# Kernel optimization log

Measured on AMD Instinct MI355X. Metric: run time of the kernel, lower is better.

The kernel has to match this reference:

```python
import jax, jax.numpy as jnp
import numpy as np

B, S, H = 1, 2048, 1024
NH, HD = 16, 64
WIN = 512
M_MEM, M_PER = 512, 64
SCALE = 1.0 / np.sqrt(HD)
NEG_INF = jnp.float32(-1e30)


def setup_inputs() -> dict:
    key = jax.random.key(0)
    ks = jax.random.split(key, 22)
    std = 1.0 / np.sqrt(H)
    def w(k):
        return (jax.random.normal(k, (H, H), jnp.float32) * std)
    names = ['local_wq','local_wk','local_wv','local_wo',
             'long_wq','long_wk','long_wv','long_wo',
             'mem_wq','mem_wk','mem_wv','mem_wo',
             'per_wq','per_wk','per_wv','per_wo']
    d = {n: w(ks[i]) for i, n in enumerate(names)}
    d['gate_w'] = jax.random.normal(ks[16], (4 * H, 4), jnp.float32) * 0.02
    d['gate_b'] = jnp.zeros((4,), jnp.float32)
    d['x'] = jax.random.normal(ks[17], (B, S, H), jnp.float32)
    d['memory_kv'] = jax.random.normal(ks[18], (B, M_MEM, H), jnp.float32)
    d['persona_kv'] = jax.random.normal(ks[19], (B, M_PER, H), jnp.float32)
    return d


def _split_heads(t):
    # (B, T, H) -> (B, NH, T, HD)
    b, t_, _ = t.shape
    return t.reshape(b, t_, NH, HD).transpose(0, 2, 1, 3)


def _merge_heads(t):
    b, h, t_, d = t.shape
    return t.transpose(0, 2, 1, 3).reshape(b, t_, h * d)


def _self_attn(x, wq, wk, wv, wo, mask):
    # mask: (S, S) bool, True = masked out
    q = _split_heads(x @ wq)
    k = _split_heads(x @ wk)
    v = _split_heads(x @ wv)
    scores = jnp.einsum('bhsd,bhtd->bhst', q, k) * SCALE
    scores = jnp.where(mask[None, None], NEG_INF, scores)
    a = jax.nn.softmax(scores, axis=-1)
    out = jnp.einsum('bhst,bhtd->bhsd', a, v)
    return _merge_heads(out) @ wo


def _cross_attn(x, ctx, wq, wk, wv, wo):
    q = _split_heads(x @ wq)
    k = _split_heads(ctx @ wk)
    v = _split_heads(ctx @ wv)
    scores = jnp.einsum('bhsd,bhmd->bhsm', q, k) * SCALE
    a = jax.nn.softmax(scores, axis=-1)
    out = jnp.einsum('bhsm,bhmd->bhsd', a, v)
    return _merge_heads(out) @ wo


def reference(x, memory_kv, persona_kv,
              local_wq, local_wk, local_wv, local_wo,
              long_wq, long_wk, long_wv, long_wo,
              mem_wq, mem_wk, mem_wv, mem_wo,
              per_wq, per_wk, per_wv, per_wo,
              gate_w, gate_b):
    s = x.shape[1]
    idx = jnp.arange(s)
    causal = idx[None, :] > idx[:, None]                    # future tokens masked
    local = causal | ((idx[:, None] - idx[None, :]) > WIN)  # sliding window + causal

    local_out = _self_attn(x, local_wq, local_wk, local_wv, local_wo, local)
    long_out = _self_attn(x, long_wq, long_wk, long_wv, long_wo, causal)
    mem_out = _cross_attn(x, memory_kv, mem_wq, mem_wk, mem_wv, mem_wo)
    per_out = _cross_attn(x, persona_kv, per_wq, per_wk, per_wv, per_wo)

    outs = (local_out, long_out, mem_out, per_out)
    gate_in = jnp.concatenate(outs, axis=-1)                # (B, S, 4H)
    gates = jax.nn.softmax(gate_in @ gate_w + gate_b, axis=-1)  # (B, S, 4)
    fused = sum(gates[..., i:i + 1] * o for i, o in enumerate(outs))
    return fused  # emotion_scale = 1.0, dropout off (eval)
```

## Files before the change

### kernel.cpp

```cpp
#include <hip/hip_runtime.h>

#define S 2048
#define H 1024
#define NH 16
#define HD 64
#define WIN 512
#define SCALE_Q 0.18033688f
#define SM_SHIFT 16.0f

typedef unsigned short u16;
typedef unsigned int u32;
typedef __attribute__((ext_vector_type(8))) short bfrag;
typedef __attribute__((ext_vector_type(4))) float facc;
typedef __attribute__((ext_vector_type(4))) unsigned short u16x4;

#define VMCNT(n) asm volatile("s_waitcnt vmcnt(" #n ")" ::: "memory")

constexpr size_t M1    = 1u << 20;
constexpr size_t WTO   = 0;
constexpr size_t XBO   = 8 * M1;
constexpr size_t MEMBO = 10 * M1;
constexpr size_t PERBO = MEMBO + (M1 >> 1);
constexpr size_t QO    = PERBO + (M1 >> 4);
constexpr size_t KVO   = QO + 8 * M1;
constexpr size_t K2O   = KVO + 8 * M1;
constexpr size_t V2O   = K2O + (M1 >> 1);
constexpr size_t K3O   = V2O + (M1 >> 1);
constexpr size_t V3O   = K3O + (M1 >> 4);
constexpr size_t VT1O  = V3O + (M1 >> 4);
constexpr size_t VT2O  = VT1O + 2 * M1;
constexpr size_t VT3O  = VT2O + (M1 >> 1);
constexpr size_t RECSZ16 = 9216;

__device__ __forceinline__ u16 f2bf(float f) {
    union { float f; unsigned u; } v; v.f = f;
    unsigned r = v.u + 0x7fffu + ((v.u >> 16) & 1u);
    return (u16)(r >> 16);
}
__device__ __forceinline__ float bf2f(u16 b) {
    union { unsigned u; float f; } v; v.u = ((unsigned)b) << 16;
    return v.f;
}
__device__ __forceinline__ void gload16(const u16* g, u16* l) {
    __builtin_amdgcn_global_load_lds(
        (const __attribute__((address_space(1))) u32*)g,
        (__attribute__((address_space(3))) u32*)l, 16, 0, 0);
}
__device__ __forceinline__ u32 cvt_pk(float a, float b) {
    u32 w;
    asm("v_cvt_pk_bf16_f32 %0, %1, %2" : "=v"(w) : "v"(a), "v"(b));
    return w;
}
__device__ __forceinline__ void blockbar() {
    __builtin_amdgcn_sched_barrier(0);
    asm volatile("" ::: "memory");
    __builtin_amdgcn_s_barrier();
    asm volatile("" ::: "memory");
    __builtin_amdgcn_sched_barrier(0);
}

__global__ __launch_bounds__(256)
void cast_all(const float* __restrict__ x, const float* __restrict__ mem,
              const float* __restrict__ per, u16* __restrict__ ws) {
    int i = blockIdx.x * 256 + threadIdx.x;
    const float* src; u16* dst;
    if (i < 262144)           { src = x;   dst = ws + XBO;   }
    else if (i < 327680)      { src = mem; dst = ws + MEMBO; i -= 262144; }
    else if (i < 335872)      { src = per; dst = ws + PERBO; i -= 327680; }
    else return;
    const float4* p = reinterpret_cast<const float4*>(src) + (size_t)i * 2;
    float4 a = p[0], b = p[1];
    u16x4 o0, o1;
    o0[0] = f2bf(a.x); o0[1] = f2bf(a.y); o0[2] = f2bf(a.z); o0[3] = f2bf(a.w);
    o1[0] = f2bf(b.x); o1[1] = f2bf(b.y); o1[2] = f2bf(b.z); o1[3] = f2bf(b.w);
    u16x4* q = reinterpret_cast<u16x4*>(dst) + (size_t)i * 2;
    q[0] = o0; q[1] = o1;
}

__global__ __launch_bounds__(256)
void transp_cast8(const float* __restrict__ w0, const float* __restrict__ w1,
                  const float* __restrict__ w2, const float* __restrict__ w3,
                  const float* __restrict__ w4, const float* __restrict__ w5,
                  const float* __restrict__ w6, const float* __restrict__ w7,
                  u16* __restrict__ wt) {
    __shared__ float t[64][65];
    const float* wp[8] = {w0, w1, w2, w3, w4, w5, w6, w7};
    const float* w = wp[blockIdx.z];
    u16* o = wt + (size_t)blockIdx.z * (1024 * 1024);
    const int kt = blockIdx.y * 64, nt = blockIdx.x * 64;
    const int r = threadIdx.x >> 4, c4 = (threadIdx.x & 15) * 4;
#pragma unroll
    for (int p = 0; p < 4; p++) {
        float4 v = *reinterpret_cast<const float4*>(
            &w[(size_t)(kt + r + p * 16) * 1024 + nt + c4]);
        t[r + p * 16][c4 + 0] = v.x; t[r + p * 16][c4 + 1] = v.y;
        t[r + p * 16][c4 + 2] = v.z; t[r + p * 16][c4 + 3] = v.w;
    }
    __syncthreads();
#pragma unroll
    for (int p = 0; p < 4; p++) {
        int nn = r + p * 16;
        u16x4 ov;
        ov[0] = f2bf(t[c4 + 0][nn]); ov[1] = f2bf(t[c4 + 1][nn]);
        ov[2] = f2bf(t[c4 + 2][nn]); ov[3] = f2bf(t[c4 + 3][nn]);
        *reinterpret_cast<u16x4*>(&o[(size_t)(nt + nn) * 1024 + kt + c4]) = ov;
    }
}

__global__ __launch_bounds__(256)
void transp_v(u16* __restrict__ ws) {
    const int z = blockIdx.z;
    const int Skv = (z < 2) ? 2048 : (z == 2 ? 512 : 64);
    const int kb = blockIdx.x;
    if (kb * 64 >= Skv) return;
    const int h = blockIdx.y;
    const u16* V = ws + (z == 0 ? KVO + 2 * M1 : z == 1 ? KVO + 6 * M1
                       : z == 2 ? V2O : V3O);
    u16* VT = ws + (z == 0 ? XBO : z == 1 ? VT1O : z == 2 ? VT2O : VT3O);
    __shared__ __align__(16) u16 t[64][72];
    {
        const int r = threadIdx.x >> 3, c8 = (threadIdx.x & 7) * 8;
#pragma unroll
        for (int p = 0; p < 2; p++) {
            int rr = r + p * 32;
            bfrag v = *reinterpret_cast<const bfrag*>(
                &V[(size_t)(kb * 64 + rr) * 1024 + h * 64 + c8]);
            *reinterpret_cast<bfrag*>(&t[rr][c8]) = v;
        }
    }
    __syncthreads();
    {
        const int d = threadIdx.x & 63;
        const int k8b = (threadIdx.x >> 6) * 8;
#pragma unroll
        for (int p = 0; p < 2; p++) {
            int k8 = k8b + p * 32;
            bfrag o;
#pragma unroll
            for (int j = 0; j < 8; j++) o[j] = (short)t[k8 + j][d];
            *reinterpret_cast<bfrag*>(
                &VT[(size_t)(h * 64 + d) * Skv + kb * 64 + k8]) = o;
        }
    }
}

__global__ __launch_bounds__(512, 2)
void gemm256(const u16* __restrict__ A, const u16* __restrict__ Bt,
             u16* __restrict__ C, long sB, long sC, int scaleMask) {
    __shared__ __align__(16) u16 sa[2][256 * 64];
    __shared__ __align__(16) u16 sb[2][256 * 64];
    Bt += (size_t)blockIdx.z * sB;
    C  += (size_t)blockIdx.z * sC;
    const float scl = ((scaleMask >> blockIdx.z) & 1) ? SCALE_Q : 1.0f;
    const int tid = threadIdx.x;
    const int wid = tid >> 6, lane = tid & 63;
    const int lhi = lane >> 4, llo = lane & 15;
    const int wm = wid >> 2, wn = wid & 3;
    const int row0 = blockIdx.y * 256, col0 = blockIdx.x * 256;

    facc acc[8][4];
#pragma unroll
    for (int i = 0; i < 8; i++)
#pragma unroll
        for (int j = 0; j < 4; j++)
#pragma unroll
            for (int k = 0; k < 4; k++) acc[i][j][k] = 0.f;

    auto stageB = [&](int kt, int h) {
        const int b = kt & 1, k0 = kt * 64;
#pragma unroll
        for (int pass = 0; pass < 2; pass++) {
            int i = pass * 512 + tid;
            int r = h * 128 + (i >> 3);
            int ck = (i & 7) ^ (r & 7);
            gload16(&Bt[(size_t)(col0 + r) * 1024 + k0 + ck * 8],
                    &sb[b][(size_t)(h * 1024 + pass * 512 + wid * 64) * 8]);
        }
    };
    auto stageAg = [&](int kt, int g) {
        const int b = kt & 1, k0 = kt * 64;
#pragma unroll
        for (int pass = 0; pass < 2; pass++) {
            int i = pass * 512 + tid;
            int i8 = i >> 3;
            int r = g * 64 + (i8 & 63) + (i8 >> 6) * 128;
            int ck = (i & 7) ^ (r & 7);
            int b8 = (pass * 512 + wid * 64) >> 3;
            int rb = g * 64 + (b8 & 63) + (b8 >> 6) * 128;
            gload16(&A[(size_t)(row0 + r) * 1024 + k0 + ck * 8],
                    &sa[b][(size_t)rb * 64]);
        }
    };

    stageB(0, 0); stageB(0, 1); stageAg(0, 0); stageAg(0, 1);
    __builtin_amdgcn_sched_barrier(0);
    VMCNT(2);
    blockbar();

    for (int j = 0; j < 16; j++) {
        const int b = j & 1;
        const u16* pa = &sa[b][0];
        const u16* pb = &sb[b][0];
        bfrag bf[4][2];
#pragma unroll
        for (int q = 0; q < 4; q++) {
            if (q == 0) {
#pragma unroll
                for (int nf = 0; nf < 4; nf++)
#pragma unroll
                    for (int ks = 0; ks < 2; ks++) {
                        int r = wn * 64 + nf * 16 + llo;
                        int p = (ks * 4 + lhi) ^ (r & 7);
                        bf[nf][ks] = *reinterpret_cast<const bfrag*>(
                            &pb[r * 64 + p * 8]);
                    }
            }
            bfrag af[2][2];
#pragma unroll
            for (int rr = 0; rr < 2; rr++)
#pragma unroll
                for (int ks = 0; ks < 2; ks++) {
                    int r = wm * 128 + (q * 2 + rr) * 16 + llo;
                    int p = (ks * 4 + lhi) ^ (r & 7);
                    af[rr][ks] = *reinterpret_cast<const bfrag*>(
                        &pa[r * 64 + p * 8]);
                }
            if (j < 15) {
                if (q == 0)      stageB(j + 1, 0);
                else if (q == 1) stageB(j + 1, 1);
                else if (q == 2) stageAg(j + 1, 0);
                else             stageAg(j + 1, 1);
            }
            blockbar();
            asm volatile("s_waitcnt lgkmcnt(0)" ::: "memory");
            __builtin_amdgcn_sched_barrier(0);
            __builtin_amdgcn_s_setprio(1);
#pragma unroll
            for (int rr = 0; rr < 2; rr++)
#pragma unroll
                for (int nf = 0; nf < 4; nf++)
#pragma unroll
                    for (int ks = 0; ks < 2; ks++)
                        acc[q * 2 + rr][nf] = __builtin_amdgcn_mfma_f32_16x16x32_bf16(
                            af[rr][ks], bf[nf][ks], acc[q * 2 + rr][nf], 0, 0, 0);
            __builtin_amdgcn_s_setprio(0);
            __builtin_amdgcn_sched_barrier(0);
            if (q == 1) { if (j < 15) { VMCNT(4); } else { VMCNT(0); } }
            else if (q == 3 && j < 15) { VMCNT(2); }
            blockbar();
        }
    }

#pragma unroll
    for (int mf = 0; mf < 8; mf++) {
#pragma unroll
        for (int r = 0; r < 4; r++) {
            int row = row0 + wm * 128 + mf * 16 + lhi * 4 + r;
#pragma unroll
            for (int nf = 0; nf < 4; nf++) {
                int col = col0 + wn * 64 + nf * 16 + llo;
                C[(size_t)row * 1024 + col] = f2bf(acc[mf][nf][r] * scl);
            }
        }
    }
}

__device__ __forceinline__ void gemm128_body(
    const u16* __restrict__ A, const u16* __restrict__ Bt, u16* __restrict__ C,
    int M, float scl, u16* sa, u16* sb, int row0, int col0) {
    const int tid = threadIdx.x;
    const int wid = tid >> 6, lane = tid & 63;
    const int lhi = lane >> 4, llo = lane & 15;
    const int wm = wid >> 1, wn = wid & 1;

    facc acc[4][4];
#pragma unroll
    for (int i = 0; i < 4; i++)
#pragma unroll
        for (int j = 0; j < 4; j++)
#pragma unroll
            for (int k = 0; k < 4; k++) acc[i][j][k] = 0.f;

    const int srow = lane >> 3, schunk = lane & 7;
    for (int kt = 0; kt < 16; kt++) {
        __syncthreads();
        const int k0 = kt * 64;
#pragma unroll
        for (int j = 0; j < 4; j++) {
            int r = wid * 32 + j * 8 + srow;
            int ck = schunk ^ (r & 7);
            int ar = row0 + r; if (ar > M - 1) ar = M - 1;
            gload16(&A[(size_t)ar * 1024 + k0 + ck * 8], &sa[(wid * 4 + j) * 512]);
            gload16(&Bt[(size_t)(col0 + r) * 1024 + k0 + ck * 8], &sb[(wid * 4 + j) * 512]);
        }
        __syncthreads();
#pragma unroll
        for (int ks = 0; ks < 2; ks++) {
            bfrag af[4], bfv[4];
#pragma unroll
            for (int mf = 0; mf < 4; mf++) {
                int r = wm * 64 + mf * 16 + llo;
                int p = (ks * 4 + lhi) ^ (r & 7);
                af[mf] = *reinterpret_cast<const bfrag*>(&sa[r * 64 + p * 8]);
            }
#pragma unroll
            for (int nf = 0; nf < 4; nf++) {
                int r = wn * 64 + nf * 16 + llo;
                int p = (ks * 4 + lhi) ^ (r & 7);
                bfv[nf] = *reinterpret_cast<const bfrag*>(&sb[r * 64 + p * 8]);
            }
            __builtin_amdgcn_s_setprio(1);
#pragma unroll
            for (int mf = 0; mf < 4; mf++)
#pragma unroll
                for (int nf = 0; nf < 4; nf++)
                    acc[mf][nf] = __builtin_amdgcn_mfma_f32_16x16x32_bf16(
                        af[mf], bfv[nf], acc[mf][nf], 0, 0, 0);
            __builtin_amdgcn_s_setprio(0);
        }
    }
#pragma unroll
    for (int mf = 0; mf < 4; mf++) {
#pragma unroll
        for (int r = 0; r < 4; r++) {
            int row = row0 + wm * 64 + mf * 16 + lhi * 4 + r;
            if (row < M) {
#pragma unroll
                for (int nf = 0; nf < 4; nf++) {
                    int col = col0 + wn * 64 + nf * 16 + llo;
                    C[(size_t)row * 1024 + col] = f2bf(acc[mf][nf][r] * scl);
                }
            }
        }
    }
}

__global__ __launch_bounds__(256)
void gemm_bf16(const u16* __restrict__ A, const u16* __restrict__ Bt,
               u16* __restrict__ C, int M, long sA, long sB, long sC,
               int scaleMask) {
    __shared__ __align__(16) u16 sa[128 * 64];
    __shared__ __align__(16) u16 sb[128 * 64];
    A  += (size_t)blockIdx.z * sA;
    Bt += (size_t)blockIdx.z * sB;
    C  += (size_t)blockIdx.z * sC;
    const float scl = ((scaleMask >> blockIdx.z) & 1) ? SCALE_Q : 1.0f;
    gemm128_body(A, Bt, C, M, scl, sa, sb, blockIdx.y * 128, blockIdx.x * 128);
}

__global__ __launch_bounds__(256)
void gemm_small(u16* __restrict__ ws) {
    const int z = blockIdx.z;
    if (z >= 2 && blockIdx.y > 0) return;
    __shared__ __align__(16) u16 sa[128 * 64];
    __shared__ __align__(16) u16 sb[128 * 64];
    const u16* A = ws + ((z < 2) ? MEMBO : PERBO);
    const int M = (z < 2) ? 512 : 64;
    const u16* Bt = ws + WTO + (size_t)z * M1;
    u16* C = ws + (z == 0 ? K2O : z == 1 ? V2O : z == 2 ? K3O : V3O);
    gemm128_body(A, Bt, C, M, 1.0f, sa, sb, blockIdx.y * 128, blockIdx.x * 128);
}

__global__ __launch_bounds__(256)
void attn_tiled(u16* __restrict__ ws) {
    __shared__ __align__(16) u16 ksm[2][64 * 64];
    __shared__ __align__(16) u16 vtm[2][64 * 64];
    __shared__ __align__(16) u16 psm[4][16][72];

    const int blk = blockIdx.x;
    int branch, h, qb, piece = 0, nway = 1, rid = -1;
    if (blk < 256)        { branch = 0; qb = 15 - (blk >> 4); h = blk & 15; }
    else if (blk < 768)   { branch = 1; int i = blk - 256; qb = 15 - (i >> 6);
                            int t = i & 63; h = t >> 2; piece = t & 3; nway = 4;
                            rid = h * 40 + 8 + (qb - 8) * 4 + piece; }
    else if (blk < 896)   { branch = 1; int i = blk - 768; qb = 7 - (i >> 5);
                            int t = i & 31; h = t >> 1; piece = t & 1; nway = 2;
                            rid = h * 40 + (qb - 4) * 2 + piece; }
    else if (blk < 960)   { branch = 1; int i = blk - 896; qb = 3 - (i >> 4); h = i & 15; }
    else if (blk < 1216)  { branch = 2; int i = blk - 960; qb = i >> 4; h = i & 15; }
    else                  { branch = 3; int i = blk - 1216; qb = i >> 4; h = i & 15; }
    const bool partial = (rid >= 0);

    size_t kb_, vb_; int Skv, maskMode;
    if (branch == 0)      { kb_ = KVO;          vb_ = XBO;  Skv = 2048; maskMode = 2; }
    else if (branch == 1) { kb_ = KVO + 4 * M1; vb_ = VT1O; Skv = 2048; maskMode = 1; }
    else if (branch == 2) { kb_ = K2O;          vb_ = VT2O; Skv = 512;  maskMode = 0; }
    else                  { kb_ = K3O;          vb_ = VT3O; Skv = 64;   maskMode = 0; }
    const u16* Kp  = ws + kb_;
    const u16* VTp = ws + vb_;
    u16* Qp = ws + QO + (size_t)branch * 2 * M1;

    const int tid = threadIdx.x, wid = tid >> 6, lane = tid & 63;
    const int llo = lane & 15, lhi = lane >> 4;
    const int q0 = qb * 128;
    const int qw = q0 + wid * 32;
    const int hoff = h * 64;

    int tBeg, tEnd;
    if (branch == 1) {
        int n = qb * 2 + 2;
        tBeg = (n * piece) / nway;
        tEnd = (n * (piece + 1)) / nway;
    } else if (branch == 0) {
        tEnd = qb * 2 + 2;
        tBeg = (q0 >= WIN) ? ((q0 - WIN) >> 6) : 0;
    } else {
        tBeg = 0; tEnd = Skv >> 6;
    }
    int myBeg = tBeg, myEnd = tEnd;
    if (maskMode) { int e = ((qw + 31) >> 6) + 1; if (e < myEnd) myEnd = e; }
    if (maskMode == 2 && qw >= WIN) { int b = (qw - WIN) >> 6; if (b > myBeg) myBeg = b; }

    bfrag qf[2][2];
#pragma unroll
    for (int sub = 0; sub < 2; sub++)
#pragma unroll
        for (int ds = 0; ds < 2; ds++)
            qf[sub][ds] = *reinterpret_cast<const bfrag*>(
                &Qp[(size_t)(qw + sub * 16 + llo) * 1024 + hoff + ds * 32 + lhi * 8]);

    facc ot[2][4];
    float lsum[2] = {0.f, 0.f};
#pragma unroll
    for (int sub = 0; sub < 2; sub++)
#pragma unroll
        for (int db = 0; db < 4; db++)
#pragma unroll
            for (int k = 0; k < 4; k++) ot[sub][db][k] = 0.f;

    const int srow = lane >> 3, schunk = lane & 7;
    auto stage = [&](int buf, int kt) {
#pragma unroll
        for (int j = 0; j < 2; j++) {
            int r = wid * 16 + j * 8 + srow;
            int ck = schunk ^ (r & 7);
            gload16(&Kp[(size_t)(kt * 64 + r) * 1024 + hoff + ck * 8],
                    &ksm[buf][(wid * 2 + j) * 512]);
            gload16(&VTp[(size_t)(hoff + r) * Skv + kt * 64 + ck * 8],
                    &vtm[buf][(wid * 2 + j) * 512]);
        }
    };

    const int nt = tEnd - tBeg;
    stage(0, tBeg);
    if (nt > 1) stage(1, tBeg + 1);
    __builtin_amdgcn_sched_barrier(0);
    if (nt > 1) { VMCNT(4); } else { VMCNT(0); }
    blockbar();

    for (int kt = tBeg; kt < tEnd; kt++) {
        const int cur = (kt - tBeg) & 1;

        if (kt >= myBeg && kt < myEnd) {
            bfrag kf[4][2], vf[4][2];
#pragma unroll
            for (int nf = 0; nf < 4; nf++)
#pragma unroll
                for (int ds = 0; ds < 2; ds++) {
                    int r = nf * 16 + llo;
                    int p = (ds * 4 + lhi) ^ (r & 7);
                    kf[nf][ds] = *reinterpret_cast<const bfrag*>(
                        &ksm[cur][r * 64 + p * 8]);
                }
#pragma unroll
            for (int db = 0; db < 4; db++)
#pragma unroll
                for (int ks = 0; ks < 2; ks++) {
                    int d = db * 16 + llo;
                    int p = (ks * 4 + lhi) ^ (d & 7);
                    vf[db][ks] = *reinterpret_cast<const bfrag*>(
                        &vtm[cur][d * 64 + p * 8]);
                }

#pragma unroll
            for (int sub = 0; sub < 2; sub++) {
                const int qsb = qw + sub * 16;
                facc st[4];
#pragma unroll
                for (int nf = 0; nf < 4; nf++)
#pragma unroll
                    for (int k = 0; k < 4; k++) st[nf][k] = 0.f;
                __builtin_amdgcn_s_setprio(1);
#pragma unroll
                for (int nf = 0; nf < 4; nf++)
#pragma unroll
                    for (int ds = 0; ds < 2; ds++)
                        st[nf] = __builtin_amdgcn_mfma_f32_16x16x32_bf16(
                            kf[nf][ds], qf[sub][ds], st[nf], 0, 0, 0);
                __builtin_amdgcn_s_setprio(0);

                float s[16];
#pragma unroll
                for (int nf = 0; nf < 4; nf++)
#pragma unroll
                    for (int r = 0; r < 4; r++) s[nf * 4 + r] = st[nf][r];

                const bool needC = maskMode && (kt * 64 + 63 > qsb);
                const bool needW = (maskMode == 2) && (kt * 64 < qsb + 15 - WIN);
                if (needC || needW) {
                    const int qi = qsb + llo;
#pragma unroll
                    for (int nf = 0; nf < 4; nf++)
#pragma unroll
                        for (int r = 0; r < 4; r++) {
                            int key = kt * 64 + nf * 16 + lhi * 4 + r;
                            if ((needC && key > qi) || (needW && (qi - key) > WIN))
                                s[nf * 4 + r] = -1e30f;
                        }
                }
                float p[16];
#pragma unroll
                for (int i = 0; i < 16; i++)
                    p[i] = __builtin_amdgcn_exp2f(s[i] - SM_SHIFT);
#pragma unroll
                for (int i = 0; i < 16; i++) lsum[sub] += p[i];

#pragma unroll
                for (int nf = 0; nf < 4; nf++)
#pragma unroll
                    for (int rp = 0; rp < 2; rp++) {
                        u32 w = cvt_pk(p[nf * 4 + rp * 2], p[nf * 4 + rp * 2 + 1]);
                        *reinterpret_cast<u32*>(
                            &psm[wid][llo][nf * 16 + lhi * 4 + rp * 2]) = w;
                    }
                bfrag pf0 = *reinterpret_cast<const bfrag*>(&psm[wid][llo][lhi * 8]);
                bfrag pf1 = *reinterpret_cast<const bfrag*>(&psm[wid][llo][32 + lhi * 8]);
                __builtin_amdgcn_s_setprio(1);
#pragma unroll
                for (int db = 0; db < 4; db++) {
                    ot[sub][db] = __builtin_amdgcn_mfma_f32_16x16x32_bf16(
                        vf[db][0], pf0, ot[sub][db], 0, 0, 0);
                    ot[sub][db] = __builtin_amdgcn_mfma_f32_16x16x32_bf16(
                        vf[db][1], pf1, ot[sub][db], 0, 0, 0);
                }
                __builtin_amdgcn_s_setprio(0);
            }
        }
        if (kt + 1 < tEnd) {
            blockbar();
            if (kt + 2 < tEnd) stage(cur, kt + 2);
            __builtin_amdgcn_sched_barrier(0);
            if (kt + 2 < tEnd) { VMCNT(4); } else { VMCNT(0); }
            blockbar();
        }
    }

    if (!partial) {
#pragma unroll
        for (int sub = 0; sub < 2; sub++) {
            float l = lsum[sub];
            l += __shfl_xor(l, 16);
            l += __shfl_xor(l, 32);
            float inv = 1.f / l;
            u16* orow = &Qp[(size_t)(qw + sub * 16 + llo) * 1024 + hoff];
#pragma unroll
            for (int db = 0; db < 4; db++) {
                u16x4 pk;
#pragma unroll
                for (int r = 0; r < 4; r++) pk[r] = f2bf(ot[sub][db][r] * inv);
                *reinterpret_cast<u16x4*>(&orow[db * 16 + lhi * 4]) = pk;
            }
        }
    } else {
        u16* rec = ws + WTO + (size_t)rid * RECSZ16;
        float* lrec = reinterpret_cast<float*>(rec + 8192);
#pragma unroll
        for (int sub = 0; sub < 2; sub++) {
            float l = lsum[sub];
            l += __shfl_xor(l, 16);
            l += __shfl_xor(l, 32);
            lrec[sub * 256 + tid] = l;
#pragma unroll
            for (int db = 0; db < 4; db++) {
                u16x4 pk;
#pragma unroll
                for (int r = 0; r < 4; r++) pk[r] = f2bf(ot[sub][db][r]);
                *reinterpret_cast<u16x4*>(&rec[tid * 32 + sub * 16 + db * 4]) = pk;
            }
        }
    }
}

__global__ __launch_bounds__(256)
void combine_split(u16* __restrict__ ws) {
    const int gi = blockIdx.x;
    const int h = gi / 12, rem = gi % 12;
    int qb, nway, rbase;
    if (rem < 4) { qb = 4 + rem; nway = 2; rbase = h * 40 + rem * 2; }
    else         { qb = 8 + (rem - 4); nway = 4; rbase = h * 40 + 8 + (rem - 4) * 4; }
    const int tid = threadIdx.x, wid = tid >> 6, lane = tid & 63;
    const int llo = lane & 15, lhi = lane >> 4;
    u16* Qp = ws + QO + 2 * M1;
    const int qw = qb * 128 + wid * 32;
#pragma unroll
    for (int sub = 0; sub < 2; sub++) {
        float l = 0.f;
        float ov[16];
#pragma unroll
        for (int i = 0; i < 16; i++) ov[i] = 0.f;
        for (int k = 0; k < nway; k++) {
            const u16* rec = ws + WTO + (size_t)(rbase + k) * RECSZ16;
            const float* lrec = reinterpret_cast<const float*>(rec + 8192);
            l += lrec[sub * 256 + tid];
#pragma unroll
            for (int i = 0; i < 16; i += 4) {
                u16x4 pk = *reinterpret_cast<const u16x4*>(
                    &rec[tid * 32 + sub * 16 + i]);
#pragma unroll
                for (int r = 0; r < 4; r++) ov[i + r] += bf2f(pk[r]);
            }
        }
        float inv = 1.f / l;
        u16* orow = &Qp[(size_t)(qw + sub * 16 + llo) * 1024 + h * 64];
#pragma unroll
        for (int db = 0; db < 4; db++) {
            u16x4 pk;
#pragma unroll
            for (int r = 0; r < 4; r++) pk[r] = f2bf(ov[db * 4 + r] * inv);
            *reinterpret_cast<u16x4*>(&orow[db * 16 + lhi * 4]) = pk;
        }
    }
}

__global__ __launch_bounds__(256)
void gate_fuse(const u16* __restrict__ o4, const float* __restrict__ gw,
               const float* __restrict__ gb, float* __restrict__ out) {
    const int s = blockIdx.x, tid = threadIdx.x;
    const u16* ob0 = o4 + (size_t)s * H;
    float p[4] = {0.f, 0.f, 0.f, 0.f};
    for (int b = 0; b < 4; b++) {
        const u16* obb = ob0 + b * 2 * M1;
        const float* gwb = gw + (size_t)b * H * 4;
        for (int i = tid; i < H; i += 256) {
            float xv = bf2f(obb[i]);
            float4 g4 = *reinterpret_cast<const float4*>(&gwb[(size_t)i * 4]);
            p[0] += xv * g4.x; p[1] += xv * g4.y;
            p[2] += xv * g4.z; p[3] += xv * g4.w;
        }
    }
#pragma unroll
    for (int off = 1; off < 64; off <<= 1)
#pragma unroll
        for (int j = 0; j < 4; j++) p[j] += __shfl_xor(p[j], off);
    __shared__ float red[4][4];
    if ((tid & 63) == 0) {
        int w = tid >> 6;
#pragma unroll
        for (int j = 0; j < 4; j++) red[w][j] = p[j];
    }
    __syncthreads();
    float gl[4];
#pragma unroll
    for (int j = 0; j < 4; j++)
        gl[j] = gb[j] + red[0][j] + red[1][j] + red[2][j] + red[3][j];
    float mx = fmaxf(fmaxf(gl[0], gl[1]), fmaxf(gl[2], gl[3]));
    float e[4]; float tot = 0.f;
#pragma unroll
    for (int j = 0; j < 4; j++) { e[j] = __expf(gl[j] - mx); tot += e[j]; }
    float inv = 1.f / tot;
    int d = tid * 4;
    float4 rv; rv.x = rv.y = rv.z = rv.w = 0.f;
#pragma unroll
    for (int b = 0; b < 4; b++) {
        const u16* obb = ob0 + b * 2 * M1 + d;
        float wgt = e[b] * inv;
        rv.x += wgt * bf2f(obb[0]);
        rv.y += wgt * bf2f(obb[1]);
        rv.z += wgt * bf2f(obb[2]);
        rv.w += wgt * bf2f(obb[3]);
    }
    *reinterpret_cast<float4*>(&out[(size_t)s * H + d]) = rv;
}

extern "C" void kernel_launch(void* const* d_in, const int* in_sizes, int n_in,
                              void* d_out, int out_size, void* d_ws, size_t ws_size,
                              hipStream_t stream) {
    const float* Wm[16];
    for (int i = 0; i < 16; i++) Wm[i] = (const float*)d_in[i];
    const float* gw = (const float*)d_in[16];
    const float* gb = (const float*)d_in[17];
    const float* x = (const float*)d_in[18];
    const float* mem = (const float*)d_in[19];
    const float* per = (const float*)d_in[20];
    float* out = (float*)d_out;
    u16* ws = (u16*)d_ws;

    dim3 blk(256);
    cast_all<<<dim3(1312), blk, 0, stream>>>(x, mem, per, ws);

    transp_cast8<<<dim3(16, 16, 8), blk, 0, stream>>>(
        Wm[0], Wm[4], Wm[8], Wm[12], Wm[1], Wm[2], Wm[5], Wm[6], ws + WTO);
    gemm256<<<dim3(4, 8, 8), dim3(512), 0, stream>>>(
        ws + XBO, ws + WTO, ws + QO, (long)M1, (long)(2 * M1), 0xF);

    transp_cast8<<<dim3(16, 16, 4), blk, 0, stream>>>(
        Wm[9], Wm[10], Wm[13], Wm[14], Wm[9], Wm[10], Wm[13], Wm[14], ws + WTO);
    gemm_small<<<dim3(8, 4, 4), blk, 0, stream>>>(ws);

    transp_v<<<dim3(32, 16, 4), blk, 0, stream>>>(ws);
    attn_tiled<<<dim3(1472), blk, 0, stream>>>(ws);
    combine_split<<<dim3(192), blk, 0, stream>>>(ws);

    transp_cast8<<<dim3(16, 16, 4), blk, 0, stream>>>(
        Wm[3], Wm[7], Wm[11], Wm[15], Wm[3], Wm[7], Wm[11], Wm[15], ws + WTO);
    gemm_bf16<<<dim3(8, 16, 4), blk, 0, stream>>>(
        ws + QO, ws + WTO, ws + KVO, 2048, (long)(2 * M1), (long)M1,
        (long)(2 * M1), 0);

    gate_fuse<<<dim3(S), blk, 0, stream>>>(ws + KVO, gw, gb, out);
}
```

Baseline: 178.8 us.

## Replace double-buffered K/V staging with single-buffer synchronous loads in attention

The attention kernel drops its two-stage LDS ping-pong for K and V^T tiles. Each iteration now loads one tile into a single buffer between two __syncthreads calls. This halves the LDS used by K/V, which may let more blocks fit per CU and removes the manual vmcnt bookkeeping. The cost is that the prefetch of the next tile no longer overlaps with the current tile's MFMA work, so global-load latency is exposed each iteration. The tile-range setup is also folded into one partial/non-partial branch.

```diff
diff --git a/kernel.cpp b/kernel.cpp
--- a/kernel.cpp
+++ b/kernel.cpp
@@ -363,8 +363,8 @@
 
 __global__ __launch_bounds__(256)
 void attn_tiled(u16* __restrict__ ws) {
-    __shared__ __align__(16) u16 ksm[2][64 * 64];
-    __shared__ __align__(16) u16 vtm[2][64 * 64];
+    __shared__ __align__(16) u16 ksm[64 * 64];
+    __shared__ __align__(16) u16 vtm[64 * 64];
     __shared__ __align__(16) u16 psm[4][16][72];
 
     const int blk = blockIdx.x;
@@ -397,15 +397,13 @@
     const int hoff = h * 64;
 
     int tBeg, tEnd;
-    if (branch == 1) {
+    if (partial) {
         int n = qb * 2 + 2;
         tBeg = (n * piece) / nway;
         tEnd = (n * (piece + 1)) / nway;
-    } else if (branch == 0) {
-        tEnd = qb * 2 + 2;
-        tBeg = (q0 >= WIN) ? ((q0 - WIN) >> 6) : 0;
     } else {
-        tBeg = 0; tEnd = Skv >> 6;
+        tEnd = maskMode ? (qb * 2 + 2) : (Skv >> 6);
+        tBeg = (maskMode == 2 && q0 >= WIN) ? ((q0 - WIN) >> 6) : 0;
     }
     int myBeg = tBeg, myEnd = tEnd;
     if (maskMode) { int e = ((qw + 31) >> 6) + 1; if (e < myEnd) myEnd = e; }
@@ -429,27 +427,19 @@
             for (int k = 0; k < 4; k++) ot[sub][db][k] = 0.f;
 
     const int srow = lane >> 3, schunk = lane & 7;
-    auto stage = [&](int buf, int kt) {
+
+    for (int kt = tBeg; kt < tEnd; kt++) {
+        __syncthreads();
 #pragma unroll
         for (int j = 0; j < 2; j++) {
             int r = wid * 16 + j * 8 + srow;
             int ck = schunk ^ (r & 7);
             gload16(&Kp[(size_t)(kt * 64 + r) * 1024 + hoff + ck * 8],
-                    &ksm[buf][(wid * 2 + j) * 512]);
+                    &ksm[(wid * 2 + j) * 512]);
             gload16(&VTp[(size_t)(hoff + r) * Skv + kt * 64 + ck * 8],
-                    &vtm[buf][(wid * 2 + j) * 512]);
-        }
-    };
-
-    const int nt = tEnd - tBeg;
-    stage(0, tBeg);
-    if (nt > 1) stage(1, tBeg + 1);
-    __builtin_amdgcn_sched_barrier(0);
-    if (nt > 1) { VMCNT(4); } else { VMCNT(0); }
-    blockbar();
-
-    for (int kt = tBeg; kt < tEnd; kt++) {
-        const int cur = (kt - tBeg) & 1;
+                    &vtm[(wid * 2 + j) * 512]);
+        }
+        __syncthreads();
 
         if (kt >= myBeg && kt < myEnd) {
             bfrag kf[4][2], vf[4][2];
@@ -460,7 +450,7 @@
                     int r = nf * 16 + llo;
                     int p = (ds * 4 + lhi) ^ (r & 7);
                     kf[nf][ds] = *reinterpret_cast<const bfrag*>(
-                        &ksm[cur][r * 64 + p * 8]);
+                        &ksm[r * 64 + p * 8]);
                 }
 #pragma unroll
             for (int db = 0; db < 4; db++)
@@ -469,7 +459,7 @@
                     int d = db * 16 + llo;
                     int p = (ks * 4 + lhi) ^ (d & 7);
                     vf[db][ks] = *reinterpret_cast<const bfrag*>(
-                        &vtm[cur][d * 64 + p * 8]);
+                        &vtm[d * 64 + p * 8]);
                 }
 
 #pragma unroll
@@ -535,13 +525,6 @@
                 }
                 __builtin_amdgcn_s_setprio(0);
             }
-        }
-        if (kt + 1 < tEnd) {
-            blockbar();
-            if (kt + 2 < tEnd) stage(cur, kt + 2);
-            __builtin_amdgcn_sched_barrier(0);
-            if (kt + 2 < tEnd) { VMCNT(4); } else { VMCNT(0); }
-            blockbar();
         }
     }
 
```

Result: no change. 178.4 us (-0.2%).
